# Kernel optimization log

Hardware: AMD Instinct MI355X
Metric: run time of the kernel (lower is better)

## Reference

```python
import jax, jax.numpy as jnp
import numpy as np


def _grid_sample_bilinear_border(img, grid):
    # img: [N, C, H, W]; grid: [N, H, W, 2] with (x, y) in [-1, 1]
    # Matches torch F.grid_sample(mode='bilinear', padding_mode='border', align_corners=False)
    N, C, H, W = img.shape
    gx, gy = grid[..., 0], grid[..., 1]
    # unnormalize (align_corners=False), then border-clip the source coords
    x = jnp.clip(((gx + 1.0) * W - 1.0) * 0.5, 0.0, W - 1.0)
    y = jnp.clip(((gy + 1.0) * H - 1.0) * 0.5, 0.0, H - 1.0)
    x0f = jnp.floor(x); y0f = jnp.floor(y)
    wx = (x - x0f)[:, None]  # [N,1,H,W]
    wy = (y - y0f)[:, None]
    x0 = x0f.astype(jnp.int32); y0 = y0f.astype(jnp.int32)
    x1 = jnp.minimum(x0 + 1, W - 1); y1 = jnp.minimum(y0 + 1, H - 1)
    imgf = img.reshape(N, C, H * W)

    def gather(yi, xi):
        idx = (yi * W + xi).reshape(N, 1, H * W)
        return jnp.take_along_axis(imgf, idx, axis=2).reshape(N, C, H, W)

    v00 = gather(y0, x0); v01 = gather(y0, x1)
    v10 = gather(y1, x0); v11 = gather(y1, x1)
    return (v00 * (1 - wx) + v01 * wx) * (1 - wy) + (v10 * (1 - wx) + v11 * wx) * wy


def setup_inputs() -> dict:
    key = jax.random.key(0)
    k1, k2, k3 = jax.random.split(key, 3)
    h_prev = jax.random.normal(k1, (4, 16, 128, 128, 64), dtype=jnp.float32)
    flow = jax.random.normal(k2, (4, 2, 128, 128), dtype=jnp.float32) * 0.1
    dt = jax.random.uniform(k3, (4,), dtype=jnp.float32)
    return {"h_prev": h_prev, "flow": flow, "dt": dt}


def reference(h_prev, flow, dt):
    # h_prev: [B, C, H, W, R], flow: [B, 2, H, W], dt: [B]
    B, C, H, W, R = h_prev.shape
    gy, gx = jnp.meshgrid(jnp.linspace(-1.0, 1.0, H, dtype=h_prev.dtype),
                          jnp.linspace(-1.0, 1.0, W, dtype=h_prev.dtype),
                          indexing='ij')
    base_grid = jnp.stack((gx, gy), axis=-1)  # [H, W, 2], (x, y)
    flow_dt = flow * dt[:, None, None, None]  # [B, 2, H, W]
    grid = base_grid[None] - jnp.transpose(flow_dt, (0, 2, 3, 1))  # [B, H, W, 2]
    # flow is shared across R, so warp all C*R channels with one grid (same math as the chunked loop)
    img = jnp.transpose(h_prev, (0, 1, 4, 2, 3)).reshape(B, C * R, H, W)
    warped = _grid_sample_bilinear_border(img, grid)
    return jnp.transpose(warped.reshape(B, C, R, H, W), (0, 1, 3, 4, 2))
```

## Files before the change

### kernel.cpp

```cpp
#include <hip/hip_runtime.h>
#include <hip/hip_bf16.h>


constexpr int B = 4, C = 16, H = 128, W = 128, R = 64;
constexpr int R4 = R / 4;
constexpr int NPIX = B * H * W;
constexpr int NXCD = 8;
constexpr int SLAB = NPIX / NXCD;

__global__ __launch_bounds__(256) void lie_transport_kernel(
    const float* __restrict__ h,
    const float* __restrict__ flow,
    const float* __restrict__ dt,
    float* __restrict__ out)
{
    const int raw  = blockIdx.x;
    const int pix  = (raw & (NXCD - 1)) * SLAB + (raw >> 3);

    const int b  = pix >> 14;
    const int yx = pix & 16383;
    const int y  = yx >> 7;
    const int x  = yx & 127;

    const float dtb = dt[b];
    const float fx = flow[((b * 2 + 0) * H + y) * W + x];
    const float fy = flow[((b * 2 + 1) * H + y) * W + x];

    const float gx = (-1.0f + 2.0f * (float)x / (float)(W - 1)) - fx * dtb;
    const float gy = (-1.0f + 2.0f * (float)y / (float)(H - 1)) - fy * dtb;

    float xs = ((gx + 1.0f) * (float)W - 1.0f) * 0.5f;
    float ys = ((gy + 1.0f) * (float)H - 1.0f) * 0.5f;
    xs = fminf(fmaxf(xs, 0.0f), (float)(W - 1));
    ys = fminf(fmaxf(ys, 0.0f), (float)(H - 1));

    const float x0f = floorf(xs);
    const float y0f = floorf(ys);
    const float wx = xs - x0f;
    const float wy = ys - y0f;
    const int x0 = (int)x0f;
    const int y0 = (int)y0f;
    const int x1 = min(x0 + 1, W - 1);
    const int y1 = min(y0 + 1, H - 1);

    const int t  = threadIdx.x;
    const int c  = t >> 4;
    const int r4 = t & 15;

    const float4* __restrict__ h4 = (const float4*)h;
    float4* __restrict__ o4 = (float4*)out;

    const int planeBase = (b * C + c) * H;

    const int i00 = ((planeBase + y0) * W + x0) * R4 + r4;
    const int i01 = ((planeBase + y0) * W + x1) * R4 + r4;
    const int i10 = ((planeBase + y1) * W + x0) * R4 + r4;
    const int i11 = ((planeBase + y1) * W + x1) * R4 + r4;

    const float4 v00 = h4[i00];
    const float4 v01 = h4[i01];
    const float4 v10 = h4[i10];
    const float4 v11 = h4[i11];

    const float w1mx = 1.0f - wx;
    const float w1my = 1.0f - wy;

    float4 r;
    r.x = (v00.x * w1mx + v01.x * wx) * w1my + (v10.x * w1mx + v11.x * wx) * wy;
    r.y = (v00.y * w1mx + v01.y * wx) * w1my + (v10.y * w1mx + v11.y * wx) * wy;
    r.z = (v00.z * w1mx + v01.z * wx) * w1my + (v10.z * w1mx + v11.z * wx) * wy;
    r.w = (v00.w * w1mx + v01.w * wx) * w1my + (v10.w * w1mx + v11.w * wx) * wy;

    o4[((planeBase + y) * W + x) * R4 + r4] = r;
}

extern "C" void kernel_launch(void* const* d_in, const int* in_sizes, int n_in,
                              void* d_out, int out_size, void* d_ws, size_t ws_size,
                              hipStream_t stream) {
    const float* h_prev = (const float*)d_in[0];
    const float* flow   = (const float*)d_in[1];
    const float* dt     = (const float*)d_in[2];
    float* out = (float*)d_out;

    lie_transport_kernel<<<NPIX, 256, 0, stream>>>(h_prev, flow, dt, out);
}
```

Before: 468.0 us.

## Process eight pixels per block with double-buffered gathers and nontemporal stores

Each block now handles eight consecutive pixels instead of one, loading flow as float4 vectors and software-pipelining the four-corner gathers two pixels ahead of the blend and store. Output is written with nontemporal stores so streaming writes do not pollute cache. This cuts block launch overhead and exposes more memory-level parallelism per thread, but it raises register pressure and reduces the grid eightfold, which may lower occupancy and latency hiding.

```diff
diff --git a/kernel.cpp b/kernel.cpp
--- a/kernel.cpp
+++ b/kernel.cpp
@@ -1,12 +1,17 @@
 #include <hip/hip_runtime.h>
-#include <hip/hip_bf16.h>
 
 
 constexpr int B = 4, C = 16, H = 128, W = 128, R = 64;
 constexpr int R4 = R / 4;
 constexpr int NPIX = B * H * W;
+constexpr int NP = 8;
+constexpr int NGRP = NPIX / NP;
 constexpr int NXCD = 8;
-constexpr int SLAB = NPIX / NXCD;
+constexpr int GSLAB = NGRP / NXCD;
+
+using vfloat4 = __attribute__((ext_vector_type(4))) float;
+
+struct Px { int i00, i01, i10, i11; float wx, wy; };
 
 __global__ __launch_bounds__(256) void lie_transport_kernel(
     const float* __restrict__ h,
@@ -15,33 +20,13 @@
     float* __restrict__ out)
 {
     const int raw  = blockIdx.x;
-    const int pix  = (raw & (NXCD - 1)) * SLAB + (raw >> 3);
+    const int grp  = (raw & (NXCD - 1)) * GSLAB + (raw >> 3);
+    const int pix0 = grp * NP;
 
-    const int b  = pix >> 14;
-    const int yx = pix & 16383;
+    const int b  = pix0 >> 14;
+    const int yx = pix0 & 16383;
     const int y  = yx >> 7;
-    const int x  = yx & 127;
-
-    const float dtb = dt[b];
-    const float fx = flow[((b * 2 + 0) * H + y) * W + x];
-    const float fy = flow[((b * 2 + 1) * H + y) * W + x];
-
-    const float gx = (-1.0f + 2.0f * (float)x / (float)(W - 1)) - fx * dtb;
-    const float gy = (-1.0f + 2.0f * (float)y / (float)(H - 1)) - fy * dtb;
-
-    float xs = ((gx + 1.0f) * (float)W - 1.0f) * 0.5f;
-    float ys = ((gy + 1.0f) * (float)H - 1.0f) * 0.5f;
-    xs = fminf(fmaxf(xs, 0.0f), (float)(W - 1));
-    ys = fminf(fmaxf(ys, 0.0f), (float)(H - 1));
-
-    const float x0f = floorf(xs);
-    const float y0f = floorf(ys);
-    const float wx = xs - x0f;
-    const float wy = ys - y0f;
-    const int x0 = (int)x0f;
-    const int y0 = (int)y0f;
-    const int x1 = min(x0 + 1, W - 1);
-    const int y1 = min(y0 + 1, H - 1);
+    const int xb = yx & 127;
 
     const int t  = threadIdx.x;
     const int c  = t >> 4;
@@ -49,29 +34,85 @@
 
     const float4* __restrict__ h4 = (const float4*)h;
     float4* __restrict__ o4 = (float4*)out;
+    const float4* __restrict__ f4 = (const float4*)flow;
+
+    const float dtb = dt[b];
+    const int fbase = (b * 2 * H + y) * W + xb;
+    const float4 fxa = f4[(fbase >> 2) + 0];
+    const float4 fxb = f4[(fbase >> 2) + 1];
+    const float4 fya = f4[((fbase + H * W) >> 2) + 0];
+    const float4 fyb = f4[((fbase + H * W) >> 2) + 1];
+
+    const float fxv[NP] = {fxa.x, fxa.y, fxa.z, fxa.w, fxb.x, fxb.y, fxb.z, fxb.w};
+    const float fyv[NP] = {fya.x, fya.y, fya.z, fya.w, fyb.x, fyb.y, fyb.z, fyb.w};
 
     const int planeBase = (b * C + c) * H;
+    const int rowOff = planeBase * W * R4 + r4;
+    const float gy0 = -1.0f + 2.0f * (float)y / (float)(H - 1);
 
-    const int i00 = ((planeBase + y0) * W + x0) * R4 + r4;
-    const int i01 = ((planeBase + y0) * W + x1) * R4 + r4;
-    const int i10 = ((planeBase + y1) * W + x0) * R4 + r4;
-    const int i11 = ((planeBase + y1) * W + x1) * R4 + r4;
+    auto coords = [&](int k) -> Px {
+        const float gx  = (-1.0f + 2.0f * (float)(xb + k) / (float)(W - 1)) - fxv[k] * dtb;
+        const float gyv = gy0 - fyv[k] * dtb;
+        float xs = ((gx  + 1.0f) * (float)W - 1.0f) * 0.5f;
+        float ys = ((gyv + 1.0f) * (float)H - 1.0f) * 0.5f;
+        xs = fminf(fmaxf(xs, 0.0f), (float)(W - 1));
+        ys = fminf(fmaxf(ys, 0.0f), (float)(H - 1));
+        const float x0f = floorf(xs);
+        const float y0f = floorf(ys);
+        Px p;
+        p.wx = xs - x0f;
+        p.wy = ys - y0f;
+        const int x0  = (int)x0f;
+        const int y0i = (int)y0f;
+        const int x1  = min(x0 + 1, W - 1);
+        const int y1  = min(y0i + 1, H - 1);
+        p.i00 = rowOff + (y0i * W + x0) * R4;
+        p.i01 = rowOff + (y0i * W + x1) * R4;
+        p.i10 = rowOff + (y1  * W + x0) * R4;
+        p.i11 = rowOff + (y1  * W + x1) * R4;
+        return p;
+    };
 
-    const float4 v00 = h4[i00];
-    const float4 v01 = h4[i01];
-    const float4 v10 = h4[i10];
-    const float4 v11 = h4[i11];
+    auto blend = [&](const Px& p, const float4& v00, const float4& v01,
+                     const float4& v10, const float4& v11) -> float4 {
+        const float w1mx = 1.0f - p.wx;
+        const float w1my = 1.0f - p.wy;
+        float4 r;
+        r.x = (v00.x * w1mx + v01.x * p.wx) * w1my + (v10.x * w1mx + v11.x * p.wx) * p.wy;
+        r.y = (v00.y * w1mx + v01.y * p.wx) * w1my + (v10.y * w1mx + v11.y * p.wx) * p.wy;
+        r.z = (v00.z * w1mx + v01.z * p.wx) * w1my + (v10.z * w1mx + v11.z * p.wx) * p.wy;
+        r.w = (v00.w * w1mx + v01.w * p.wx) * w1my + (v10.w * w1mx + v11.w * p.wx) * p.wy;
+        return r;
+    };
 
-    const float w1mx = 1.0f - wx;
-    const float w1my = 1.0f - wy;
+    auto store_nt = [&](const float4& v, float4* dst) {
+        vfloat4 nv;
+        nv.x = v.x; nv.y = v.y; nv.z = v.z; nv.w = v.w;
+        __builtin_nontemporal_store(nv, (vfloat4*)dst);
+    };
 
-    float4 r;
-    r.x = (v00.x * w1mx + v01.x * wx) * w1my + (v10.x * w1mx + v11.x * wx) * wy;
-    r.y = (v00.y * w1mx + v01.y * wx) * w1my + (v10.y * w1mx + v11.y * wx) * wy;
-    r.z = (v00.z * w1mx + v01.z * wx) * w1my + (v10.z * w1mx + v11.z * wx) * wy;
-    r.w = (v00.w * w1mx + v01.w * wx) * w1my + (v10.w * w1mx + v11.w * wx) * wy;
+    const int obase = ((planeBase + y) * W + xb) * R4 + r4;
 
-    o4[((planeBase + y) * W + x) * R4 + r4] = r;
+    Px pA = coords(0);
+    float4 a00 = h4[pA.i00], a01 = h4[pA.i01], a10 = h4[pA.i10], a11 = h4[pA.i11];
+    Px pB = coords(1);
+    float4 b00 = h4[pB.i00], b01 = h4[pB.i01], b10 = h4[pB.i10], b11 = h4[pB.i11];
+
+    #pragma unroll
+    for (int k = 0; k < NP; k += 2) {
+        const float4 rA = blend(pA, a00, a01, a10, a11);
+        store_nt(rA, &o4[obase + k * R4]);
+        if (k + 2 < NP) {
+            pA = coords(k + 2);
+            a00 = h4[pA.i00]; a01 = h4[pA.i01]; a10 = h4[pA.i10]; a11 = h4[pA.i11];
+        }
+        const float4 rB = blend(pB, b00, b01, b10, b11);
+        store_nt(rB, &o4[obase + (k + 1) * R4]);
+        if (k + 3 < NP) {
+            pB = coords(k + 3);
+            b00 = h4[pB.i00]; b01 = h4[pB.i01]; b10 = h4[pB.i10]; b11 = h4[pB.i11];
+        }
+    }
 }
 
 extern "C" void kernel_launch(void* const* d_in, const int* in_sizes, int n_in,
@@ -82,5 +123,5 @@
     const float* dt     = (const float*)d_in[2];
     float* out = (float*)d_out;
 
-    lie_transport_kernel<<<NPIX, 256, 0, stream>>>(h_prev, flow, dt, out);
+    lie_transport_kernel<<<NGRP, 256, 0, stream>>>(h_prev, flow, dt, out);
 }
```

Result: no change. 468.4 us (+0.1%).
